# Optimization experiments

Hardware: AMD Instinct MI355X
Metric: run time of the kernel (lower is better)

The kernel has to match this reference:

```python
import jax, jax.numpy as jnp
import numpy as np
import math

NUM_HEADS = 16
KV_HEADS = 4
WINDOW = 1024  # sliding_window

def _alibi_slopes(n):
    # n is a power of 2 here (16)
    start = 2.0 ** (-(2.0 ** (-(math.log2(n) - 3))))
    return jnp.array([start * (start ** i) for i in range(n)], dtype=jnp.float32)

def setup_inputs() -> dict:
    key = jax.random.key(0)
    k0, k1, k2, k3, k4 = jax.random.split(key, 5)
    B, S, H = 2, 2048, 2048
    D = H // NUM_HEADS
    std = 0.02
    return {
        "hidden_states": jax.random.normal(k0, (B, S, H), dtype=jnp.float32),
        "Wq": jax.random.normal(k1, (H, H), dtype=jnp.float32) * std,
        "Wk": jax.random.normal(k2, (H, KV_HEADS * D), dtype=jnp.float32) * std,
        "Wv": jax.random.normal(k3, (H, KV_HEADS * D), dtype=jnp.float32) * std,
        "Wo": jax.random.normal(k4, (H, H), dtype=jnp.float32) * std,
    }

def reference(hidden_states, Wq, Wk, Wv, Wo):
    B, S, H = hidden_states.shape
    D = H // NUM_HEADS
    g = NUM_HEADS // KV_HEADS  # query groups per kv head

    q = (hidden_states @ Wq).reshape(B, S, NUM_HEADS, D).transpose(0, 2, 1, 3)  # [B,Hq,S,D]
    k = (hidden_states @ Wk).reshape(B, S, KV_HEADS, D).transpose(0, 2, 1, 3)   # [B,Hkv,S,D]
    v = (hidden_states @ Wv).reshape(B, S, KV_HEADS, D).transpose(0, 2, 1, 3)

    # GQA head expansion: each kv head repeated g times (matches expand+flatten order)
    k = jnp.repeat(k, g, axis=1)  # [B,Hq,S,D]
    v = jnp.repeat(v, g, axis=1)

    i = jnp.arange(S)[:, None]
    j = jnp.arange(S)[None, :]

    # ALiBi bias: -clamp(j - i, min=0) * slope_h  (faithful to source, incl. its quirk)
    dist = -jnp.clip(j - i, 0, None).astype(jnp.float32)          # [S,S]
    alibi = dist[None, :, :] * _alibi_slopes(NUM_HEADS)[:, None, None]  # [H,S,S]

    # Sliding window mask (kv_seq_len=S > WINDOW): True on [i-W, i] -> 1.0, else -1e9
    window = (j <= i) & (j >= i - WINDOW)
    sliding = jnp.where(window, 1.0, -1e9).astype(jnp.float32)    # [S,S]

    scores = jnp.einsum('bhqd,bhkd->bhqk', q, k) * (1.0 / math.sqrt(D))
    scores = scores + alibi[None] + sliding[None, None]
    # Causal mask (past_kv is None): strictly-upper triangle -> -inf
    scores = jnp.where((j > i)[None, None], -jnp.inf, scores)

    w = jax.nn.softmax(scores, axis=-1)  # dropout is identity in eval
    out = jnp.einsum('bhqk,bhkd->bhqd', w, v)          # [B,H,S,D]
    out = out.transpose(0, 2, 1, 3).reshape(B, S, H)    # [B,S,hidden]
    return out @ Wo
```

## Files before the change

kernel.cpp:

```cpp
#include <hip/hip_runtime.h>
#include <stdint.h>

typedef unsigned short u16;
typedef unsigned short bf16x8 __attribute__((ext_vector_type(8)));
typedef unsigned short u16x4 __attribute__((ext_vector_type(4)));
typedef float f32x4 __attribute__((ext_vector_type(4)));

typedef __attribute__((address_space(3))) unsigned int lds_u32;
typedef __attribute__((address_space(1))) unsigned int gbl_u32;

__device__ __forceinline__ u16 f2bf(float f) {
    unsigned u = __builtin_bit_cast(unsigned, f);
    u += 0x7fffu + ((u >> 16) & 1u);
    return (u16)(u >> 16);
}

__device__ __forceinline__ void mfma_bf16(f32x4& d, bf16x8 a, bf16x8 b) {
    asm("v_mfma_f32_16x16x32_bf16 %0, %1, %2, %0" : "+v"(d) : "v"(a), "v"(b));
}

__device__ __forceinline__ void g2l16(const void* g, void* l) {
    unsigned int loff = (unsigned int)(unsigned long long)l;
    __builtin_amdgcn_global_load_lds(
        reinterpret_cast<gbl_u32*>((unsigned long long)g),
        reinterpret_cast<lds_u32*>(loff), 16, 0, 0);
}

__global__ __launch_bounds__(256) void cast_bf16_kernel(const float* __restrict__ in,
                                                        u16* __restrict__ out, int n) {
    int i = (blockIdx.x * 256 + threadIdx.x) * 4;
    if (i >= n) return;
    f32x4 v = *reinterpret_cast<const f32x4*>(in + i);
    u16x4 o;
#pragma unroll
    for (int k = 0; k < 4; k++) o[k] = f2bf(v[k]);
    *reinterpret_cast<u16x4*>(out + i) = o;
}

__global__ __launch_bounds__(256) void transpose_cast_kernel(const float* __restrict__ W,
                                                             u16* __restrict__ Wt, int K, int N) {
    __shared__ float tile[32][33];
    int n0 = blockIdx.x * 32, k0 = blockIdx.y * 32;
    int tx = threadIdx.x, ty = threadIdx.y;
#pragma unroll
    for (int i = 0; i < 4; i++)
        tile[ty + i * 8][tx] = W[(size_t)(k0 + ty + i * 8) * N + n0 + tx];
    __syncthreads();
#pragma unroll
    for (int i = 0; i < 4; i++)
        Wt[(size_t)(n0 + ty + i * 8) * K + k0 + tx] = f2bf(tile[tx][ty + i * 8]);
}

__global__ __launch_bounds__(256) void vt_transpose_kernel(const u16* __restrict__ KV,
                                                           u16* __restrict__ Vt) {
    __shared__ u16 tile[32][33];
    int s0 = blockIdx.x * 32, d0 = blockIdx.y * 32, bh = blockIdx.z;
    int b = bh >> 2, hkv = bh & 3;
    int tx = threadIdx.x, ty = threadIdx.y;
#pragma unroll
    for (int i = 0; i < 4; i++) {
        int s = s0 + ty + i * 8;
        tile[ty + i * 8][tx] = KV[(size_t)(b * 2048 + s) * 1024 + 512 + hkv * 128 + d0 + tx];
    }
    __syncthreads();
#pragma unroll
    for (int i = 0; i < 4; i++) {
        int d = d0 + ty + i * 8;
        Vt[((size_t)bh * 128 + d) * 2048 + s0 + tx] = tile[tx][ty + i * 8];
    }
}

template <int OF32>
__global__ __launch_bounds__(256) void gemm_bt_kernel(const u16* __restrict__ A,
                                                      const u16* __restrict__ Bt,
                                                      void* __restrict__ Cout,
                                                      int M, int N, int K) {
    __shared__ u16 lA[128 * 32];
    __shared__ u16 lB[128 * 32];
    int n0 = blockIdx.x * 128, m0 = blockIdx.y * 128;
    int t = threadIdx.x, w = t >> 6, l = t & 63;
    int wm = w >> 1, wn = w & 1;
    int lg = l >> 4, lc = l & 15;

    f32x4 acc[4][4] = {};

    const char* Ab = (const char*)A;
    const char* Bb = (const char*)Bt;

    for (int kt = 0; kt < K; kt += 32) {
        __syncthreads();
#pragma unroll
        for (int i = 0; i < 2; i++) {
            int r = (i * 256 + t) >> 2;
            int innerb = (t & 3) * 16;
            g2l16(Ab + ((size_t)(m0 + r) * K + kt) * 2 + innerb, lA + (i * 256 + w * 64) * 8);
            g2l16(Bb + ((size_t)(n0 + r) * K + kt) * 2 + innerb, lB + (i * 256 + w * 64) * 8);
        }
        __syncthreads();

        bf16x8 af[4], bf[4];
        int ko = lg * 8;
#pragma unroll
        for (int fm = 0; fm < 4; fm++)
            af[fm] = *(const bf16x8*)(lA + (wm * 64 + fm * 16 + lc) * 32 + ko);
#pragma unroll
        for (int fn = 0; fn < 4; fn++)
            bf[fn] = *(const bf16x8*)(lB + (wn * 64 + fn * 16 + lc) * 32 + ko);
#pragma unroll
        for (int fm = 0; fm < 4; fm++)
#pragma unroll
            for (int fn = 0; fn < 4; fn++)
                mfma_bf16(acc[fm][fn], af[fm], bf[fn]);
    }
    asm volatile("s_nop 7\n s_nop 7\n s_nop 7" ::);

#pragma unroll
    for (int fm = 0; fm < 4; fm++)
#pragma unroll
        for (int fn = 0; fn < 4; fn++)
#pragma unroll
            for (int j = 0; j < 4; j++) {
                int r = m0 + wm * 64 + fm * 16 + lg * 4 + j;
                int c = n0 + wn * 64 + fn * 16 + lc;
                if (OF32)
                    ((float*)Cout)[(size_t)r * N + c] = acc[fm][fn][j];
                else
                    ((u16*)Cout)[(size_t)r * N + c] = f2bf(acc[fm][fn][j]);
            }
}

__global__ __launch_bounds__(256) void attn_kernel(const u16* __restrict__ Q,
                                                   const u16* __restrict__ KV,
                                                   const u16* __restrict__ Vt,
                                                   u16* __restrict__ AO) {
    __shared__ u16 lK[64 * 128];
    __shared__ u16 lV[128 * 64];
    __shared__ u16 lP[4 * 16 * 64];

    int bid = blockIdx.x;
    int qt = bid & 31, h = (bid >> 5) & 15, b = bid >> 9;
    int hkv = h >> 2;
    int q0 = qt * 64;
    int t = threadIdx.x, w = t >> 6, l = t & 63;
    int lg = l >> 4, lc = l & 15;

    bf16x8 qf[4];
    {
        const u16* qrow = Q + (size_t)(b * 2048 + q0 + w * 16 + lc) * 2048 + h * 128;
#pragma unroll
        for (int ks = 0; ks < 4; ks++)
            qf[ks] = *(const bf16x8*)(qrow + ks * 32 + lg * 8);
    }

    f32x4 acc[8] = {};
    float mrow[4], lrow[4];
#pragma unroll
    for (int j = 0; j < 4; j++) { mrow[j] = -INFINITY; lrow[j] = 0.0f; }

    int t0 = (qt > 16) ? (qt - 16) : 0;
    for (int kt = t0; kt <= qt; kt++) {
        int ks0 = kt * 64;
        __syncthreads();
#pragma unroll
        for (int i = 0; i < 4; i++) {
            int L = (i * 256 + t) * 16;
            int r = L >> 8, inner = L & 255;
            const char* g = (const char*)KV +
                ((size_t)(b * 2048 + ks0 + r) * 1024 + hkv * 128) * 2 + (inner ^ ((r & 7) << 4));
            g2l16(g, (char*)lK + (i * 256 + w * 64) * 16);
        }
#pragma unroll
        for (int i = 0; i < 4; i++) {
            int L = (i * 256 + t) * 16;
            int r = L >> 7, inner = L & 127;
            const char* g = (const char*)Vt +
                ((size_t)((b * 4 + hkv) * 128 + r) * 2048 + ks0) * 2 + (inner ^ ((r & 7) << 4));
            g2l16(g, (char*)lV + (i * 256 + w * 64) * 16);
        }
        __syncthreads();

        f32x4 sacc[4] = {};
        asm volatile("s_nop 7" ::);
#pragma unroll
        for (int fn = 0; fn < 4; fn++) {
#pragma unroll
            for (int ks = 0; ks < 4; ks++) {
                int srow = fn * 16 + lc;
                int boff = (ks * 64 + lg * 16) ^ ((srow & 7) << 4);
                bf16x8 kf = *(const bf16x8*)((const char*)lK + srow * 256 + boff);
                mfma_bf16(sacc[fn], qf[ks], kf);
            }
        }
        asm volatile("s_nop 7\n s_nop 7" ::);

        float p[4][4];
#pragma unroll
        for (int j = 0; j < 4; j++) {
            int qrow = q0 + w * 16 + lg * 4 + j;
            float sv[4];
            float mx = -INFINITY;
#pragma unroll
            for (int fn = 0; fn < 4; fn++) {
                int key = ks0 + fn * 16 + lc;
                float s = sacc[fn][j] * 0.08838834764831845f;
                bool valid = (key <= qrow) && (key + 1024 >= qrow);
                sv[fn] = valid ? s : -INFINITY;
                mx = fmaxf(mx, sv[fn]);
            }
#pragma unroll
            for (int m = 1; m < 16; m <<= 1) mx = fmaxf(mx, __shfl_xor(mx, m, 64));
            float mnew = fmaxf(mrow[j], mx);
            float muse = fmaxf(mnew, -1e30f);
            float fac = __expf(mrow[j] - muse);
            mrow[j] = mnew;
            float psum = 0.0f;
#pragma unroll
            for (int fn = 0; fn < 4; fn++) {
                float pv = __expf(sv[fn] - muse);
                p[fn][j] = pv;
                psum += pv;
            }
#pragma unroll
            for (int m = 1; m < 16; m <<= 1) psum += __shfl_xor(psum, m, 64);
            lrow[j] = lrow[j] * fac + psum;
#pragma unroll
            for (int fn = 0; fn < 8; fn++) acc[fn][j] *= fac;
        }

#pragma unroll
        for (int fn = 0; fn < 4; fn++)
#pragma unroll
            for (int j = 0; j < 4; j++) {
                int r = lg * 4 + j;
                int cb = (fn * 16 + lc) * 2;
                *(u16*)((char*)lP + w * 2048 + r * 128 + (cb ^ ((r & 7) << 4))) = f2bf(p[fn][j]);
            }
        __syncthreads();

        asm volatile("s_nop 7" ::);
#pragma unroll
        for (int kk = 0; kk < 2; kk++) {
            int pboff = (kk * 64 + lg * 16) ^ ((lc & 7) << 4);
            bf16x8 pf = *(const bf16x8*)((const char*)lP + w * 2048 + lc * 128 + pboff);
#pragma unroll
            for (int fn = 0; fn < 8; fn++) {
                int vrow = fn * 16 + lc;
                int vboff = (kk * 64 + lg * 16) ^ ((vrow & 7) << 4);
                bf16x8 vf = *(const bf16x8*)((const char*)lV + vrow * 128 + vboff);
                mfma_bf16(acc[fn], pf, vf);
            }
        }
    }
    asm volatile("s_nop 7\n s_nop 7" ::);

#pragma unroll
    for (int j = 0; j < 4; j++) {
        float inv = 1.0f / lrow[j];
        size_t base = (size_t)(b * 2048 + q0 + w * 16 + lg * 4 + j) * 2048 + h * 128;
#pragma unroll
        for (int fn = 0; fn < 8; fn++)
            AO[base + fn * 16 + lc] = f2bf(acc[fn][j] * inv);
    }
}

extern "C" void kernel_launch(void* const* d_in, const int* in_sizes, int n_in,
                              void* d_out, int out_size, void* d_ws, size_t ws_size,
                              hipStream_t stream) {
    const float* hs = (const float*)d_in[0];
    const float* Wq = (const float*)d_in[1];
    const float* Wk = (const float*)d_in[2];
    const float* Wv = (const float*)d_in[3];
    const float* Wo = (const float*)d_in[4];
    float* out = (float*)d_out;

    u16* ws = (u16*)d_ws;
    u16* hsB  = ws;
    u16* WqT  = hsB + 8388608;
    u16* WkvT = WqT + 4194304;
    u16* WoT  = WkvT + 2097152;
    u16* Qb   = WoT + 4194304;
    u16* KVb  = Qb + 8388608;
    u16* Vtb  = WqT;
    u16* AOb  = hsB;

    cast_bf16_kernel<<<8192, 256, 0, stream>>>(hs, hsB, 8388608);
    transpose_cast_kernel<<<dim3(64, 64), dim3(32, 8), 0, stream>>>(Wq, WqT, 2048, 2048);
    transpose_cast_kernel<<<dim3(16, 64), dim3(32, 8), 0, stream>>>(Wk, WkvT, 2048, 512);
    transpose_cast_kernel<<<dim3(16, 64), dim3(32, 8), 0, stream>>>(Wv, WkvT + (size_t)512 * 2048, 2048, 512);
    transpose_cast_kernel<<<dim3(64, 64), dim3(32, 8), 0, stream>>>(Wo, WoT, 2048, 2048);

    gemm_bt_kernel<0><<<dim3(16, 32), 256, 0, stream>>>(hsB, WqT, Qb, 4096, 2048, 2048);
    gemm_bt_kernel<0><<<dim3(8, 32), 256, 0, stream>>>(hsB, WkvT, KVb, 4096, 1024, 2048);

    vt_transpose_kernel<<<dim3(64, 4, 8), dim3(32, 8), 0, stream>>>(KVb, Vtb);

    attn_kernel<<<1024, 256, 0, stream>>>(Qb, KVb, Vtb, AOb);

    gemm_bt_kernel<1><<<dim3(16, 32), 256, 0, stream>>>(AOb, WoT, out, 4096, 2048, 2048);
}
```

Baseline: 260.1 us.

## Read K/V fragments directly from global memory and swizzle block order for L2 locality

The attention kernel drops the shared-memory staging of K and V tiles and the block-wide barriers, so each wave loads its MFMA operand fragments straight from global memory (relying on L2/L1 caching) and only uses a wave-local wait for its private P tile. Attention blocks are remapped so the heaviest query tiles start first and blocks sharing a KV head are spread across XCDs, and the GEMM grid gets a similar XCD-aware tile swizzle. This removes barrier and LDS copy overhead but duplicates K/V global traffic across the four waves and relies on cache hits for reuse.

```diff
diff --git a/kernel.cpp b/kernel.cpp
--- a/kernel.cpp
+++ b/kernel.cpp
@@ -77,7 +77,12 @@
                                                       int M, int N, int K) {
     __shared__ u16 lA[128 * 32];
     __shared__ u16 lB[128 * 32];
-    int n0 = blockIdx.x * 128, m0 = blockIdx.y * 128;
+    int nbx = gridDim.x;
+    int nwg = nbx * gridDim.y;
+    int lin = blockIdx.y * nbx + blockIdx.x;
+    int swz = (lin & 7) * (nwg >> 3) + (lin >> 3);
+    int n0 = (swz % nbx) * 128, m0 = (swz / nbx) * 128;
+
     int t = threadIdx.x, w = t >> 6, l = t & 63;
     int wm = w >> 1, wn = w & 1;
     int lg = l >> 4, lc = l & 15;
@@ -133,12 +138,12 @@
                                                    const u16* __restrict__ KV,
                                                    const u16* __restrict__ Vt,
                                                    u16* __restrict__ AO) {
-    __shared__ u16 lK[64 * 128];
-    __shared__ u16 lV[128 * 64];
     __shared__ u16 lP[4 * 16 * 64];
 
     int bid = blockIdx.x;
-    int qt = bid & 31, h = (bid >> 5) & 15, b = bid >> 9;
+    int sb = (bid & 7) * 128 + (bid >> 3);
+    int qt = 31 - (sb & 31);
+    int h = (sb >> 5) & 15, b = sb >> 9;
     int hkv = h >> 2;
     int q0 = qt * 64;
     int t = threadIdx.x, w = t >> 6, l = t & 63;
@@ -158,26 +163,12 @@
     for (int j = 0; j < 4; j++) { mrow[j] = -INFINITY; lrow[j] = 0.0f; }
 
     int t0 = (qt > 16) ? (qt - 16) : 0;
+
+    const u16* Kb = KV + (size_t)(b * 2048) * 1024 + hkv * 128;
+    const u16* Vb = Vt + (size_t)(b * 4 + hkv) * 128 * 2048;
+
     for (int kt = t0; kt <= qt; kt++) {
         int ks0 = kt * 64;
-        __syncthreads();
-#pragma unroll
-        for (int i = 0; i < 4; i++) {
-            int L = (i * 256 + t) * 16;
-            int r = L >> 8, inner = L & 255;
-            const char* g = (const char*)KV +
-                ((size_t)(b * 2048 + ks0 + r) * 1024 + hkv * 128) * 2 + (inner ^ ((r & 7) << 4));
-            g2l16(g, (char*)lK + (i * 256 + w * 64) * 16);
-        }
-#pragma unroll
-        for (int i = 0; i < 4; i++) {
-            int L = (i * 256 + t) * 16;
-            int r = L >> 7, inner = L & 127;
-            const char* g = (const char*)Vt +
-                ((size_t)((b * 4 + hkv) * 128 + r) * 2048 + ks0) * 2 + (inner ^ ((r & 7) << 4));
-            g2l16(g, (char*)lV + (i * 256 + w * 64) * 16);
-        }
-        __syncthreads();
 
         f32x4 sacc[4] = {};
         asm volatile("s_nop 7" ::);
@@ -185,9 +176,7 @@
         for (int fn = 0; fn < 4; fn++) {
 #pragma unroll
             for (int ks = 0; ks < 4; ks++) {
-                int srow = fn * 16 + lc;
-                int boff = (ks * 64 + lg * 16) ^ ((srow & 7) << 4);
-                bf16x8 kf = *(const bf16x8*)((const char*)lK + srow * 256 + boff);
+                bf16x8 kf = *(const bf16x8*)(Kb + (size_t)(ks0 + fn * 16 + lc) * 1024 + ks * 32 + lg * 8);
                 mfma_bf16(sacc[fn], qf[ks], kf);
             }
         }
@@ -235,7 +224,8 @@
                 int cb = (fn * 16 + lc) * 2;
                 *(u16*)((char*)lP + w * 2048 + r * 128 + (cb ^ ((r & 7) << 4))) = f2bf(p[fn][j]);
             }
-        __syncthreads();
+        asm volatile("s_waitcnt lgkmcnt(0)" ::: "memory");
+        __builtin_amdgcn_sched_barrier(0);
 
         asm volatile("s_nop 7" ::);
 #pragma unroll
@@ -244,12 +234,11 @@
             bf16x8 pf = *(const bf16x8*)((const char*)lP + w * 2048 + lc * 128 + pboff);
 #pragma unroll
             for (int fn = 0; fn < 8; fn++) {
-                int vrow = fn * 16 + lc;
-                int vboff = (kk * 64 + lg * 16) ^ ((vrow & 7) << 4);
-                bf16x8 vf = *(const bf16x8*)((const char*)lV + vrow * 128 + vboff);
+                bf16x8 vf = *(const bf16x8*)(Vb + (size_t)(fn * 16 + lc) * 2048 + ks0 + kk * 32 + lg * 8);
                 mfma_bf16(acc[fn], pf, vf);
             }
         }
+        asm volatile("s_nop 7" ::);
     }
     asm volatile("s_nop 7\n s_nop 7" ::);
 
```

Result: slower. 428.7 us (+64.8%).
